# Kernel optimization log

Measured on AMD Instinct MI355X. Metric: run time of the kernel, lower is better.

Reference implementation:

```python
import jax, jax.numpy as jnp
import numpy as np

KSIZE = 5
STRIDE = 5  # == KSIZE, padding 0: unfold is an exact non-overlapping tiling


def setup_inputs() -> dict:
    key = jax.random.key(0)
    x = jax.random.normal(key, (4, 3, 320, 320), dtype=jnp.float32)
    return {"input": x}


def _extract_patches(x, k):
    # torch.nn.Unfold(k, 1, 0, k) on (n,c,h,w): channel dim ordered (c, ki, kj),
    # spatial positions row-major -> (n, L, c*k*k)
    n, c, h, w = x.shape
    hp, wp = h // k, w // k
    p = x.reshape(n, c, hp, k, wp, k)
    p = jnp.transpose(p, (0, 2, 4, 1, 3, 5))  # (n, hp, wp, c, k, k)
    return p.reshape(n, hp * wp, c * k * k), hp, wp


def reference(input):
    # DotP branch, sigmoid=True, target=None (self-match)
    p, hp, wp = _extract_patches(input, KSIZE)          # (n, L, K)
    n, L, _ = p.shape
    # per-sample scalar: max over patches of patch L2 norm
    max_wi = jnp.max(jnp.sqrt(jnp.sum(p * p, axis=-1)), axis=1)  # (n,)
    # conv2d(xi, wi/max_wi, stride=k) == patch Gram matrix / max_wi
    match = jnp.einsum('bpk,bqk->bpq', p, p) / max_wi[:, None, None]  # (n, L, L)
    match = match.reshape(n, L, hp, wp)
    return jax.nn.sigmoid(match)
```

## Files before the change

kernel.cpp:

```cpp
#include <hip/hip_runtime.h>
#include <hip/hip_bf16.h>

#define NB   4
#define CCH  3
#define HW   320
#define KS   5
#define LP   4096
#define KD   75
#define NCH  12

typedef __attribute__((ext_vector_type(4))) float f32x4;
typedef __attribute__((ext_vector_type(8))) short bf16x8;

__device__ __forceinline__ ushort f2bf(float v) {
    __hip_bfloat16 h = __float2bfloat16(v);
    return __builtin_bit_cast(ushort, h);
}

__global__ __launch_bounds__(256) void norm_kernel(const float* __restrict__ x,
                                                   float* __restrict__ blockmax) {
    int tid  = threadIdx.x;
    int lane = tid & 63;
    int pid  = blockIdx.x * 4 + (tid >> 6);
    int b    = pid >> 12;
    int pp   = pid & 4095;
    int ph   = pp >> 6, pw = pp & 63;
    const float* xb = x + (size_t)b * (CCH * HW * HW);
    int row0 = ph * KS, col0 = pw * KS;

    float ss = 0.f;
    for (int k = lane; k < KD; k += 64) {
        int c = k / 25, rem = k % 25;
        int ki = rem / 5, kj = rem % 5;
        float v = xb[(c * HW + row0 + ki) * HW + col0 + kj];
        ss += v * v;
    }
    for (int off = 32; off; off >>= 1) ss += __shfl_xor(ss, off, 64);

    __shared__ float sm[4];
    if (lane == 0) sm[tid >> 6] = ss;
    __syncthreads();
    if (tid == 0)
        blockmax[blockIdx.x] = fmaxf(fmaxf(sm[0], sm[1]), fmaxf(sm[2], sm[3]));
}

__global__ __launch_bounds__(256) void reduce_kernel(const float* __restrict__ blockmax,
                                                     float* __restrict__ invmax) {
    int b = blockIdx.x;
    float m = 0.f;
    for (int i = threadIdx.x; i < 1024; i += 256) m = fmaxf(m, blockmax[b * 1024 + i]);
    for (int off = 32; off; off >>= 1) m = fmaxf(m, __shfl_xor(m, off, 64));
    __shared__ float sm[4];
    if ((threadIdx.x & 63) == 0) sm[threadIdx.x >> 6] = m;
    __syncthreads();
    if (threadIdx.x == 0)
        invmax[b] = 1.0f / sqrtf(fmaxf(fmaxf(sm[0], sm[1]), fmaxf(sm[2], sm[3])));
}

__global__ __launch_bounds__(256) void patch_kernel(const float* __restrict__ x,
                                                    ushort* __restrict__ p2) {
    int tid = threadIdx.x;
    int r   = blockIdx.x * 256 + tid;
    int c   = blockIdx.y;
    int b   = blockIdx.z;
    int ph = r >> 6, pw = r & 63;
    const float* xb = x + (size_t)b * (CCH * HW * HW);

    bf16x8 v = {};
    if (c < 10) {
        #pragma unroll
        for (int j = 0; j < 8; ++j) {
            int k = c * 8 + j;
            float f = 0.f;
            if (k < KD) {
                int ch = k / 25, rem = k % 25;
                int ki = rem / 5, kj = rem % 5;
                f = xb[(ch * HW + ph * KS + ki) * HW + pw * KS + kj];
            }
            v[j] = (short)f2bf(f);
        }
    }
    *(bf16x8*)&p2[((size_t)(b * NCH + c) * LP + r) * 8] = v;
}

__global__ __launch_bounds__(256) void gemm_kernel(const ushort* __restrict__ p2,
                                                   const float* __restrict__ invmax,
                                                   float* __restrict__ out) {
    __shared__ float W[32][256];

    int b  = blockIdx.z;
    int ti = blockIdx.x;
    int tj = blockIdx.y;
    int tid = threadIdx.x;
    int lane = tid & 63;
    int w    = tid >> 6;
    int lrow = lane & 15;
    int lch  = lane >> 4;

    const ushort* pb = p2 + (size_t)b * NCH * LP * 8;
    int i0 = ti * 256 + w * 64;
    int j0 = tj * 64;

    f32x4 acc[4][4] = {};
    #pragma unroll
    for (int ks = 0; ks < 3; ++ks) {
        const ushort* pk = pb + (size_t)(ks * 4 + lch) * LP * 8;
        bf16x8 af[4], bfr[4];
        #pragma unroll
        for (int m = 0; m < 4; ++m)
            af[m] = *(const bf16x8*)&pk[(size_t)(i0 + m * 16 + lrow) * 8];
        #pragma unroll
        for (int n = 0; n < 4; ++n)
            bfr[n] = *(const bf16x8*)&pk[(size_t)(j0 + n * 16 + lrow) * 8];
        #pragma unroll
        for (int m = 0; m < 4; ++m)
            #pragma unroll
            for (int n = 0; n < 4; ++n)
                acc[m][n] = __builtin_amdgcn_mfma_f32_16x16x32_bf16(af[m], bfr[n], acc[m][n], 0, 0, 0);
    }

    float inv = invmax[b];
    float* ob = out + (size_t)b * LP * LP;

    #pragma unroll
    for (int h = 0; h < 2; ++h) {
        if (h) __syncthreads();
        #pragma unroll
        for (int np = 0; np < 2; ++np) {
            int n  = h * 2 + np;
            int jr = np * 16 + lrow;
            #pragma unroll
            for (int m = 0; m < 4; ++m) {
                int sl = w * 16 + (((m * 4 + lch) ^ (jr & 7)) & 15);
                f32x4 v;
                #pragma unroll
                for (int r = 0; r < 4; ++r) {
                    float s = acc[m][n][r] * inv;
                    v[r] = 1.0f / (1.0f + __expf(-s));
                }
                *(f32x4*)&W[jr][sl * 4] = v;
            }
        }
        __syncthreads();
        #pragma unroll
        for (int r8 = 0; r8 < 8; ++r8) {
            int row = w * 8 + r8;
            f32x4 v = *(const f32x4*)&W[row][(lane ^ (row & 7)) * 4];
            *(f32x4*)&ob[(size_t)(j0 + h * 32 + row) * LP + ti * 256 + lane * 4] = v;
        }
    }
}

extern "C" void kernel_launch(void* const* d_in, const int* in_sizes, int n_in,
                              void* d_out, int out_size, void* d_ws, size_t ws_size,
                              hipStream_t stream) {
    const float* x = (const float*)d_in[0];
    float* out = (float*)d_out;

    ushort* p2 = (ushort*)d_ws;
    float* blockmax = (float*)((char*)d_ws + (size_t)NB * NCH * LP * 16);
    float* invmax = blockmax + 4096;

    norm_kernel<<<(NB * LP) / 4, 256, 0, stream>>>(x, blockmax);
    patch_kernel<<<dim3(LP / 256, NCH, NB), 256, 0, stream>>>(x, p2);
    reduce_kernel<<<NB, 256, 0, stream>>>(blockmax, invmax);
    gemm_kernel<<<dim3(16, 64, NB), 256, 0, stream>>>(p2, invmax, out);
}
```

Measured before the change: 64.65 us.

## Compute patch norms from bf16 patch buffer and use nontemporal output stores

The norm kernel previously ran one wavefront per patch, reading strided fp32 input. It is replaced by a kernel that reads the packed bf16 patch buffer, one thread per patch, and reduces to 16 block maxima per sample, which shrinks the final reduce. The GEMM output stores become nontemporal to avoid cache pollution on the large 256MB output. The norm is now computed from bf16-rounded values, which slightly changes the scaling compared with fp32, and it must now run after patch_kernel.

```diff
diff --git a/kernel.cpp b/kernel.cpp
--- a/kernel.cpp
+++ b/kernel.cpp
@@ -15,46 +15,6 @@
 __device__ __forceinline__ ushort f2bf(float v) {
     __hip_bfloat16 h = __float2bfloat16(v);
     return __builtin_bit_cast(ushort, h);
-}
-
-__global__ __launch_bounds__(256) void norm_kernel(const float* __restrict__ x,
-                                                   float* __restrict__ blockmax) {
-    int tid  = threadIdx.x;
-    int lane = tid & 63;
-    int pid  = blockIdx.x * 4 + (tid >> 6);
-    int b    = pid >> 12;
-    int pp   = pid & 4095;
-    int ph   = pp >> 6, pw = pp & 63;
-    const float* xb = x + (size_t)b * (CCH * HW * HW);
-    int row0 = ph * KS, col0 = pw * KS;
-
-    float ss = 0.f;
-    for (int k = lane; k < KD; k += 64) {
-        int c = k / 25, rem = k % 25;
-        int ki = rem / 5, kj = rem % 5;
-        float v = xb[(c * HW + row0 + ki) * HW + col0 + kj];
-        ss += v * v;
-    }
-    for (int off = 32; off; off >>= 1) ss += __shfl_xor(ss, off, 64);
-
-    __shared__ float sm[4];
-    if (lane == 0) sm[tid >> 6] = ss;
-    __syncthreads();
-    if (tid == 0)
-        blockmax[blockIdx.x] = fmaxf(fmaxf(sm[0], sm[1]), fmaxf(sm[2], sm[3]));
-}
-
-__global__ __launch_bounds__(256) void reduce_kernel(const float* __restrict__ blockmax,
-                                                     float* __restrict__ invmax) {
-    int b = blockIdx.x;
-    float m = 0.f;
-    for (int i = threadIdx.x; i < 1024; i += 256) m = fmaxf(m, blockmax[b * 1024 + i]);
-    for (int off = 32; off; off >>= 1) m = fmaxf(m, __shfl_xor(m, off, 64));
-    __shared__ float sm[4];
-    if ((threadIdx.x & 63) == 0) sm[threadIdx.x >> 6] = m;
-    __syncthreads();
-    if (threadIdx.x == 0)
-        invmax[b] = 1.0f / sqrtf(fmaxf(fmaxf(sm[0], sm[1]), fmaxf(sm[2], sm[3])));
 }
 
 __global__ __launch_bounds__(256) void patch_kernel(const float* __restrict__ x,
@@ -81,6 +41,42 @@
         }
     }
     *(bf16x8*)&p2[((size_t)(b * NCH + c) * LP + r) * 8] = v;
+}
+
+__global__ __launch_bounds__(256) void normb_kernel(const ushort* __restrict__ p2,
+                                                    float* __restrict__ blockmax) {
+    int b = blockIdx.y;
+    int r = blockIdx.x * 256 + threadIdx.x;
+    const ushort* pb = p2 + (size_t)b * NCH * LP * 8;
+
+    float ss = 0.f;
+    #pragma unroll
+    for (int c = 0; c < 10; ++c) {
+        bf16x8 v = *(const bf16x8*)&pb[((size_t)c * LP + r) * 8];
+        #pragma unroll
+        for (int j = 0; j < 8; ++j) {
+            float f = __uint_as_float(((unsigned)(ushort)v[j]) << 16);
+            ss = fmaf(f, f, ss);
+        }
+    }
+    for (int off = 32; off; off >>= 1) ss = fmaxf(ss, __shfl_xor(ss, off, 64));
+    __shared__ float sm[4];
+    if ((threadIdx.x & 63) == 0) sm[threadIdx.x >> 6] = ss;
+    __syncthreads();
+    if (threadIdx.x == 0)
+        blockmax[b * 16 + blockIdx.x] =
+            fmaxf(fmaxf(sm[0], sm[1]), fmaxf(sm[2], sm[3]));
+}
+
+__global__ __launch_bounds__(64) void reduce_kernel(const float* __restrict__ blockmax,
+                                                    float* __restrict__ invmax) {
+    int b = blockIdx.x;
+    if (threadIdx.x == 0) {
+        float m = 0.f;
+        #pragma unroll
+        for (int i = 0; i < 16; ++i) m = fmaxf(m, blockmax[b * 16 + i]);
+        invmax[b] = 1.0f / sqrtf(m);
+    }
 }
 
 __global__ __launch_bounds__(256) void gemm_kernel(const ushort* __restrict__ p2,
@@ -146,7 +142,8 @@
         for (int r8 = 0; r8 < 8; ++r8) {
             int row = w * 8 + r8;
             f32x4 v = *(const f32x4*)&W[row][(lane ^ (row & 7)) * 4];
-            *(f32x4*)&ob[(size_t)(j0 + h * 32 + row) * LP + ti * 256 + lane * 4] = v;
+            __builtin_nontemporal_store(v,
+                (f32x4*)&ob[(size_t)(j0 + h * 32 + row) * LP + ti * 256 + lane * 4]);
         }
     }
 }
@@ -159,10 +156,10 @@
 
     ushort* p2 = (ushort*)d_ws;
     float* blockmax = (float*)((char*)d_ws + (size_t)NB * NCH * LP * 16);
-    float* invmax = blockmax + 4096;
+    float* invmax = blockmax + 64;
 
-    norm_kernel<<<(NB * LP) / 4, 256, 0, stream>>>(x, blockmax);
     patch_kernel<<<dim3(LP / 256, NCH, NB), 256, 0, stream>>>(x, p2);
-    reduce_kernel<<<NB, 256, 0, stream>>>(blockmax, invmax);
+    normb_kernel<<<dim3(LP / 256, NB), 256, 0, stream>>>(p2, blockmax);
+    reduce_kernel<<<NB, 64, 0, stream>>>(blockmax, invmax);
     gemm_kernel<<<dim3(16, 64, NB), 256, 0, stream>>>(p2, invmax, out);
 }
```

After: 62.74 us. 1.03x faster.
